# Kernel optimization log

Measured on AMD Instinct MI355X. Metric: run time of the kernel, lower is better.

The kernel has to match this reference:

```python
import jax, jax.numpy as jnp
import numpy as np

N, TP, E = 8, 2048, 4096
S = 8            # 2**spatial_dim
C = 64           # sqrt(embed_dim)
T = TP * S       # 16384
V = 16           # num_vocab


def setup_inputs() -> dict:
    key = jax.random.key(0)
    ks = jax.random.split(key, 9)
    x = jax.random.normal(ks[0], (N, TP, E), dtype=jnp.float32)
    value = jax.random.randint(ks[1], (N, T), 0, 4, dtype=jnp.int64)
    depth = jnp.sort(jax.random.randint(ks[2], (N, T), 0, 16, dtype=jnp.int64), axis=1)
    pos = jax.random.randint(ks[3], (N, T, 3), 0, 32, dtype=jnp.int64)
    # ConvTranspose1d(E, C, kernel=S, stride=S): weight [E, C, S]
    W1 = jax.random.normal(ks[4], (E, C, S), dtype=jnp.float32) / np.sqrt(E)
    b1 = jax.random.normal(ks[5], (C,), dtype=jnp.float32) * 0.01
    # ConvTranspose1d(C, 1, kernel=S, stride=S): weight [C, 1, S]
    W2 = jax.random.normal(ks[6], (C, 1, S), dtype=jnp.float32) / np.sqrt(C)
    b2 = jax.random.normal(ks[7], (1,), dtype=jnp.float32) * 0.01
    # Linear(1, V+1, bias=False): weight [V+1, 1]
    W3 = jax.random.normal(ks[8], (V + 1, 1), dtype=jnp.float32)
    return {"x": x, "value": value, "depth": depth, "pos": pos,
            "W1": W1, "b1": b1, "W2": W2, "b2": b2, "W3": W3}


def reference(x, value, depth, pos, W1, b1, W2, b2, W3):
    n, tp, e = x.shape
    s = W1.shape[2]
    t = value.shape[1]  # = tp * s
    posn = jnp.arange(t)
    # Truncate each value sequence at argmax(depth); pad_sequence pads with 0.
    idx = jnp.argmax(depth, axis=1)                      # [N]
    val_pad = jnp.where(posn[None, :] < idx[:, None], value, 0)  # [N, T]
    # deconv_1: stride == kernel -> non-overlapping expansion
    x1 = jnp.einsum('nte,ecs->ntsc', x, W1).reshape(n, t, -1) + b1  # [N, T, C]
    # Per-sample masked gather (val==2), compacted to front, zero-padded
    mask = val_pad == 2                                   # [N, T]
    order = jnp.argsort(jnp.logical_not(mask), axis=1, stable=True)  # True first
    y = jnp.take_along_axis(x1, order[:, :, None], axis=1)           # [N, T, C]
    counts = mask.sum(axis=1)                             # [N]
    y = jnp.where((posn[None, :] < counts[:, None])[:, :, None], y, 0.0)
    # deconv_2: [N, T, C] -> [N, T*S, 1]
    y2 = jnp.einsum('ntc,cs->nts', y, W2[:, 0, :]).reshape(n, t * s, 1) + b2
    # linear (no bias): [N, T*S, V+1]
    return y2 @ W3.T
```

## Files before the change

kernel.cpp:

```cpp
#include <hip/hip_runtime.h>

#define N_    8
#define TP_   2048
#define E_    4096
#define S_    8
#define C_    64
#define T_    16384
#define TS_   131072
#define OUTW  17
#define OUT_ELEMS 17825792
#define F4_PER_N 557056
#define F4_TOTAL 4456448

typedef __attribute__((ext_vector_type(8))) short short8;
typedef __attribute__((ext_vector_type(4))) float float4v;

static __device__ __forceinline__ unsigned short f2bf(float f) {
    unsigned int u = __builtin_bit_cast(unsigned int, f);
    u += 0x7FFFu + ((u >> 16) & 1u);
    return (unsigned short)(u >> 16);
}

__global__ __launch_bounds__(256) void prep_kernel(
    const float* __restrict__ W1, const float* __restrict__ b1,
    const float* __restrict__ W2, const float* __restrict__ b2,
    unsigned short* __restrict__ Bb, float* __restrict__ K2)
{
    __shared__ float tile[64][65];
    const int tid = threadIdx.x;
    if (blockIdx.x == 0 && blockIdx.y == 0 && tid < 8) {
        int s2 = tid;
        float acc = b2[0];
        for (int c = 0; c < C_; ++c) acc += b1[c] * W2[c * S_ + s2];
        K2[s2] = acc;
    }
    const int e0  = blockIdx.x * 64;
    const int cs0 = blockIdx.y * 64;
    {
        int rr = tid >> 2;
        int c4 = tid & 3;
        for (int i = 0; i < 4; ++i) {
            int f4 = c4 + i * 4;
            float4 v = *(const float4*)&W1[(size_t)(e0 + rr) * 512 + cs0 + f4 * 4];
            tile[f4 * 4 + 0][rr] = v.x;
            tile[f4 * 4 + 1][rr] = v.y;
            tile[f4 * 4 + 2][rr] = v.z;
            tile[f4 * 4 + 3][rr] = v.w;
        }
    }
    __syncthreads();
    {
        int cs  = tid >> 2;
        int seg = tid & 3;
        for (int h = 0; h < 2; ++h) {
            short8 o;
#pragma unroll
            for (int j = 0; j < 8; ++j)
                o[j] = (short)f2bf(tile[cs][seg * 16 + h * 8 + j]);
            *(short8*)&Bb[(size_t)(cs0 + cs) * E_ + e0 + seg * 16 + h * 8] = o;
        }
    }
}

__global__ __launch_bounds__(256) void compact_kernel(
    const int* __restrict__ value, const int* __restrict__ depth,
    int* __restrict__ cnt_ns, int* __restrict__ cnt_total,
    int* __restrict__ tile_counter, int* __restrict__ tiles,
    int* __restrict__ sel_tp, int* __restrict__ sel_j)
{
    const int g = blockIdx.x;
    const int n = g >> 3;
    const int s = g & 7;
    const int tid  = threadIdx.x;
    const int lane = tid & 63;
    const int wv   = tid >> 6;

    __shared__ int idx_sh;
    __shared__ unsigned int wsum[4];

    const int* d = depth + (size_t)n * T_;
    if (tid < 64) {
        int maxv = d[T_ - 1];
        int lower = 0, upper = T_ - 1;
        for (int rnd = 0; rnd < 3; ++rnd) {
            int span = upper - lower;
            int step = (span + 63) >> 6;
            if (step < 1) step = 1;
            int p = lower + lane * step;
            if (p > upper) p = upper;
            unsigned long long b = __ballot(d[p] == maxv);
            int f = __ffsll((long long)b) - 1;
            int nu = lower + f * step; if (nu > upper) nu = upper;
            int nl = (f == 0) ? lower : lower + (f - 1) * step + 1;
            if (nl > nu) nl = nu;
            lower = nl; upper = nu;
        }
        if (lane == 0) idx_sh = lower;
    }
    __syncthreads();
    const int idx = idx_sh;
    const int* val = value + (size_t)n * T_;

    const int t0 = tid * 64;
    unsigned int packed = 0;
    for (int i = 0; i < 64; ++i) {
        int t = t0 + i;
        if (t < idx && val[t] == 2) {
            packed += 0x10000u;
            if ((t & 7) == s) packed += 1u;
        }
    }
    unsigned int inc = packed;
#pragma unroll
    for (int off = 1; off < 64; off <<= 1) {
        unsigned int u = __shfl_up((int)inc, off, 64);
        if (lane >= off) inc += u;
    }
    if (lane == 63) wsum[wv] = inc;
    __syncthreads();
    unsigned int woff = 0;
    for (int ww = 0; ww < wv; ++ww) woff += wsum[ww];
    unsigned int excl = woff + inc - packed;
    int any_rank = (int)(excl >> 16);
    int s_rank   = (int)(excl & 0xFFFFu);
    for (int i = 0; i < 64; ++i) {
        int t = t0 + i;
        if (t < idx && val[t] == 2) {
            if ((t & 7) == s) {
                sel_tp[g * 2048 + s_rank] = t >> 3;
                sel_j [g * 2048 + s_rank] = any_rank;
                ++s_rank;
            }
            ++any_rank;
        }
    }
    if (tid == 255) {
        unsigned int tot = woff + inc;
        int cnt = (int)(tot & 0xFFFFu);
        cnt_ns[g] = cnt;
        if (s == 0) cnt_total[n] = (int)(tot >> 16);
        int ntl = (cnt + 63) >> 6;
        int base = atomicAdd(tile_counter, ntl);
        for (int i = 0; i < ntl; ++i) tiles[base + i] = (g << 8) | i;
    }
}

__global__ __launch_bounds__(256) void fill_kernel(
    float* __restrict__ out, const float* __restrict__ W3,
    const float* __restrict__ b2, const int* __restrict__ cnt_total)
{
    __shared__ float pat[136];
    const int tid = threadIdx.x;
    if (tid < 136) pat[tid] = b2[0] * W3[tid % OUTW];
    __syncthreads();
    int i4 = blockIdx.x * 256 + tid;
    int n   = i4 / F4_PER_N;
    int rem = i4 - n * F4_PER_N;
    int j   = rem / 34;
    if (j >= cnt_total[n]) {
        int o = (rem - j * 34) * 4;
        float4 v = { pat[o], pat[o + 1], pat[o + 2], pat[o + 3] };
        *(float4*)&out[(size_t)i4 * 4] = v;
    }
}

__global__ __launch_bounds__(256) void main_kernel(
    const float* __restrict__ x, const unsigned short* __restrict__ Bb,
    const int* __restrict__ tile_counter, const int* __restrict__ tiles,
    const int* __restrict__ cnt_ns, const int* __restrict__ sel_tp,
    const int* __restrict__ sel_j, const float* __restrict__ K2,
    const float* __restrict__ W2, const float* __restrict__ W3,
    float* __restrict__ out)
{
    __shared__ __align__(16) char arena[36864];
    unsigned short (*bufA)[64][72] = (unsigned short (*)[64][72])arena;
    unsigned short (*bufB)[64][72] = (unsigned short (*)[64][72])(arena + 18432);
    float (*Cl)[68] = (float (*)[68])arena;
    __shared__ int tp_l[64], j_l[64];
    __shared__ float W2s[C_ * S_];
    __shared__ float W3s[OUTW];
    __shared__ float K2s[S_];

    const int tid = threadIdx.x;
    for (int i = tid; i < C_ * S_; i += 256) W2s[i] = W2[i];
    if (tid < OUTW) W3s[tid] = W3[tid];
    if (tid < S_)   K2s[tid] = K2[tid];

    const int ntile = *tile_counter;

    const int lane = tid & 63;
    const int w    = tid >> 6;
    const int m    = lane & 15;
    const int q    = lane >> 4;
    const int r    = tid >> 4;
    const int kq   = (tid & 15) << 2;

    for (int ti = blockIdx.x; ti < ntile; ti += gridDim.x) {
        const int ent = tiles[ti];
        const int g = ent >> 8;
        const int n = g >> 3;
        const int s = g & 7;
        const int m0 = (ent & 255) * 64;
        const int rows = min(64, cnt_ns[g] - m0);

        __syncthreads();
        if (tid < 64) {
            int tp = 0, j = 0;
            if (tid < rows) {
                tp = sel_tp[g * 2048 + m0 + tid];
                j  = sel_j [g * 2048 + m0 + tid];
            }
            tp_l[tid] = tp;
            j_l[tid]  = j;
        }
        __syncthreads();

        const float* ap[4];
        const unsigned short* bp[4];
#pragma unroll
        for (int l = 0; l < 4; ++l) {
            int row = r + (l << 4);
            ap[l] = x + ((size_t)n * TP_ + tp_l[row]) * E_ + kq;
            bp[l] = Bb + ((size_t)(row * 8 + s)) * E_ + kq;
        }

        float4  Af[4];
        ushort4 Bf[4];
#pragma unroll
        for (int l = 0; l < 4; ++l) {
            Af[l] = *(const float4*)(ap[l]);
            Bf[l] = *(const ushort4*)(bp[l]);
        }

        float4v acc[4];
#pragma unroll
        for (int nt = 0; nt < 4; ++nt) acc[nt] = (float4v){0.f, 0.f, 0.f, 0.f};

        for (int kb = 0; kb < 64; ++kb) {
            const int p = kb & 1;
#pragma unroll
            for (int l = 0; l < 4; ++l) {
                int row = r + (l << 4);
                ushort4 av;
                av.x = f2bf(Af[l].x); av.y = f2bf(Af[l].y);
                av.z = f2bf(Af[l].z); av.w = f2bf(Af[l].w);
                *(ushort4*)&bufA[p][row][kq] = av;
                *(ushort4*)&bufB[p][row][kq] = Bf[l];
            }
            __syncthreads();
            if (kb < 63) {
                const int k0 = (kb + 1) * 64;
#pragma unroll
                for (int l = 0; l < 4; ++l) {
                    Af[l] = *(const float4*)(ap[l] + k0);
                    Bf[l] = *(const ushort4*)(bp[l] + k0);
                }
            }
#pragma unroll
            for (int ks = 0; ks < 2; ++ks) {
                short8 a = *(const short8*)&bufA[p][w * 16 + m][ks * 32 + q * 8];
#pragma unroll
                for (int nt = 0; nt < 4; ++nt) {
                    short8 b = *(const short8*)&bufB[p][nt * 16 + m][ks * 32 + q * 8];
                    acc[nt] = __builtin_amdgcn_mfma_f32_16x16x32_bf16(a, b, acc[nt], 0, 0, 0);
                }
            }
        }
        __syncthreads();

#pragma unroll
        for (int nt = 0; nt < 4; ++nt)
#pragma unroll
            for (int rr = 0; rr < 4; ++rr)
                Cl[w * 16 + q * 4 + rr][nt * 16 + m] = acc[nt][rr];
        __syncthreads();

        for (int task = tid; task < 512; task += 256) {
            int row = task >> 3;
            int s2  = task & 7;
            if (row < rows) {
                float y2 = K2s[s2];
#pragma unroll
                for (int c = 0; c < C_; ++c) y2 += Cl[row][c] * W2s[c * S_ + s2];
                float* o = out + ((size_t)n * TS_ + (size_t)j_l[row] * S_ + s2) * OUTW;
#pragma unroll
                for (int v = 0; v < OUTW; ++v) o[v] = y2 * W3s[v];
            }
        }
    }
}

extern "C" void kernel_launch(void* const* d_in, const int* in_sizes, int n_in,
                              void* d_out, int out_size, void* d_ws, size_t ws_size,
                              hipStream_t stream) {
    const float* x     = (const float*)d_in[0];
    const int*   value = (const int*)d_in[1];
    const int*   depth = (const int*)d_in[2];
    const float* W1    = (const float*)d_in[4];
    const float* b1    = (const float*)d_in[5];
    const float* W2    = (const float*)d_in[6];
    const float* b2    = (const float*)d_in[7];
    const float* W3    = (const float*)d_in[8];
    float* out = (float*)d_out;

    unsigned short* Bb = (unsigned short*)d_ws;
    float* K2          = (float*)(Bb + 512 * 4096);
    int* tile_counter  = (int*)(K2 + 8);
    int* cnt_ns        = tile_counter + 1;
    int* cnt_total     = cnt_ns + 64;
    int* tiles         = cnt_total + 8;
    int* sel_tp        = tiles + 2048;
    int* sel_j         = sel_tp + 64 * 2048;

    hipMemsetAsync(tile_counter, 0, sizeof(int), stream);

    dim3 pgrid(64, 8);
    prep_kernel<<<pgrid, 256, 0, stream>>>(W1, b1, W2, b2, Bb, K2);
    compact_kernel<<<64, 256, 0, stream>>>(value, depth, cnt_ns, cnt_total,
                                           tile_counter, tiles, sel_tp, sel_j);
    fill_kernel<<<F4_TOTAL / 256, 256, 0, stream>>>(out, W3, b2, cnt_total);
    main_kernel<<<1024, 256, 0, stream>>>(x, Bb, tile_counter, tiles, cnt_ns,
                                          sel_tp, sel_j, K2, W2, W3, out);
}
```

Measured before the change: 459.1 us.

## Vectorize mask scan, deepen GEMM prefetch, and write output rows as float4

The selection kernel now reads the value array as int4 instead of scalar ints. The GEMM main loop prefetches two k-blocks ahead using a two-slot register buffer, to hide more global load latency. The epilogue first computes the deconv_2 results into shared memory, then writes each output row's 136 floats as coalesced float4 stores instead of 17 scalar stores per element. The register buffer is indexed by kb&1 inside a loop that is not unrolled, which risks spilling to scratch. The extra barrier and staging also add some overhead.

```diff
diff --git a/kernel.cpp b/kernel.cpp
--- a/kernel.cpp
+++ b/kernel.cpp
@@ -99,16 +99,17 @@
     }
     __syncthreads();
     const int idx = idx_sh;
-    const int* val = value + (size_t)n * T_;
-
-    const int t0 = tid * 64;
+    const int4* val4 = (const int4*)(value + (size_t)n * T_);
+
+    const int b4 = tid * 16;
     unsigned int packed = 0;
-    for (int i = 0; i < 64; ++i) {
-        int t = t0 + i;
-        if (t < idx && val[t] == 2) {
-            packed += 0x10000u;
-            if ((t & 7) == s) packed += 1u;
-        }
+    for (int i = 0; i < 16; ++i) {
+        int4 v = val4[b4 + i];
+        int t = (b4 + i) * 4;
+        if (t + 0 < idx && v.x == 2) { packed += 0x10000u; if (((t + 0) & 7) == s) packed += 1u; }
+        if (t + 1 < idx && v.y == 2) { packed += 0x10000u; if (((t + 1) & 7) == s) packed += 1u; }
+        if (t + 2 < idx && v.z == 2) { packed += 0x10000u; if (((t + 2) & 7) == s) packed += 1u; }
+        if (t + 3 < idx && v.w == 2) { packed += 0x10000u; if (((t + 3) & 7) == s) packed += 1u; }
     }
     unsigned int inc = packed;
 #pragma unroll
@@ -123,15 +124,21 @@
     unsigned int excl = woff + inc - packed;
     int any_rank = (int)(excl >> 16);
     int s_rank   = (int)(excl & 0xFFFFu);
-    for (int i = 0; i < 64; ++i) {
-        int t = t0 + i;
-        if (t < idx && val[t] == 2) {
-            if ((t & 7) == s) {
-                sel_tp[g * 2048 + s_rank] = t >> 3;
-                sel_j [g * 2048 + s_rank] = any_rank;
-                ++s_rank;
-            }
-            ++any_rank;
+    for (int i = 0; i < 16; ++i) {
+        int4 v = val4[b4 + i];
+        int vv[4] = { v.x, v.y, v.z, v.w };
+        int t = (b4 + i) * 4;
+#pragma unroll
+        for (int e = 0; e < 4; ++e) {
+            int tt = t + e;
+            if (tt < idx && vv[e] == 2) {
+                if ((tt & 7) == s) {
+                    sel_tp[g * 2048 + s_rank] = tt >> 3;
+                    sel_j [g * 2048 + s_rank] = any_rank;
+                    ++s_rank;
+                }
+                ++any_rank;
+            }
         }
     }
     if (tid == 255) {
@@ -176,6 +183,7 @@
     unsigned short (*bufA)[64][72] = (unsigned short (*)[64][72])arena;
     unsigned short (*bufB)[64][72] = (unsigned short (*)[64][72])(arena + 18432);
     float (*Cl)[68] = (float (*)[68])arena;
+    float (*y2s)[8] = (float (*)[8])(arena + 17408);
     __shared__ int tp_l[64], j_l[64];
     __shared__ float W2s[C_ * S_];
     __shared__ float W3s[OUTW];
@@ -224,13 +232,15 @@
             bp[l] = Bb + ((size_t)(row * 8 + s)) * E_ + kq;
         }
 
-        float4  Af[4];
-        ushort4 Bf[4];
-#pragma unroll
-        for (int l = 0; l < 4; ++l) {
-            Af[l] = *(const float4*)(ap[l]);
-            Bf[l] = *(const ushort4*)(bp[l]);
-        }
+        float4  Af[2][4];
+        ushort4 Bf[2][4];
+#pragma unroll
+        for (int pp = 0; pp < 2; ++pp)
+#pragma unroll
+            for (int l = 0; l < 4; ++l) {
+                Af[pp][l] = *(const float4*)(ap[l] + pp * 64);
+                Bf[pp][l] = *(const ushort4*)(bp[l] + pp * 64);
+            }
 
         float4v acc[4];
 #pragma unroll
@@ -242,18 +252,18 @@
             for (int l = 0; l < 4; ++l) {
                 int row = r + (l << 4);
                 ushort4 av;
-                av.x = f2bf(Af[l].x); av.y = f2bf(Af[l].y);
-                av.z = f2bf(Af[l].z); av.w = f2bf(Af[l].w);
+                av.x = f2bf(Af[p][l].x); av.y = f2bf(Af[p][l].y);
+                av.z = f2bf(Af[p][l].z); av.w = f2bf(Af[p][l].w);
                 *(ushort4*)&bufA[p][row][kq] = av;
-                *(ushort4*)&bufB[p][row][kq] = Bf[l];
+                *(ushort4*)&bufB[p][row][kq] = Bf[p][l];
             }
             __syncthreads();
-            if (kb < 63) {
-                const int k0 = (kb + 1) * 64;
+            if (kb < 62) {
+                const int k0 = (kb + 2) * 64;
 #pragma unroll
                 for (int l = 0; l < 4; ++l) {
-                    Af[l] = *(const float4*)(ap[l] + k0);
-                    Bf[l] = *(const ushort4*)(bp[l] + k0);
+                    Af[p][l] = *(const float4*)(ap[l] + k0);
+                    Bf[p][l] = *(const ushort4*)(bp[l] + k0);
                 }
             }
 #pragma unroll
@@ -278,13 +288,27 @@
         for (int task = tid; task < 512; task += 256) {
             int row = task >> 3;
             int s2  = task & 7;
+            float y2 = K2s[s2];
+#pragma unroll
+            for (int c = 0; c < C_; ++c) y2 += Cl[row][c] * W2s[c * S_ + s2];
+            y2s[row][s2] = y2;
+        }
+        __syncthreads();
+
+        for (int task = tid; task < 64 * 34; task += 256) {
+            int row = task / 34;
+            int f   = task - row * 34;
             if (row < rows) {
-                float y2 = K2s[s2];
-#pragma unroll
-                for (int c = 0; c < C_; ++c) y2 += Cl[row][c] * W2s[c * S_ + s2];
-                float* o = out + ((size_t)n * TS_ + (size_t)j_l[row] * S_ + s2) * OUTW;
-#pragma unroll
-                for (int v = 0; v < OUTW; ++v) o[v] = y2 * W3s[v];
+                float4 v;
+                float* vp = (float*)&v;
+#pragma unroll
+                for (int e = 0; e < 4; ++e) {
+                    int idx = f * 4 + e;
+                    int s2  = (idx * 241) >> 12;
+                    int vi  = idx - s2 * OUTW;
+                    vp[e] = y2s[row][s2] * W3s[vi];
+                }
+                *(float4*)&out[((size_t)n * TS_ + (size_t)j_l[row] * S_) * OUTW + f * 4] = v;
             }
         }
     }
```

New measurement: 690.1 us. +50.3%, slower.
